# Optimization experiments

Hardware: AMD Instinct MI355X
Metric: run time of the kernel (lower is better)

## Reference

```python
import jax, jax.numpy as jnp
import numpy as np

B, C, T = 32, 64, 1024        # batch_size, in_channels, cycle_size
H, D = 2, 64                  # GATv2 heads, per-head dim (dim_h)
DIM2 = H * D                  # dim_h * 2 = 128
K = 9                         # temporal_kernel_size
N = B * T                     # graph nodes after flatten
E = 524288                    # edges (avg degree 16)
EPS = 1e-5


def bn3d(x, gamma, beta):
    # BatchNorm1d on [B, C, T] in training mode (batch statistics)
    mu = x.mean(axis=(0, 2), keepdims=True)
    var = x.var(axis=(0, 2), keepdims=True)
    xn = (x - mu) * jax.lax.rsqrt(var + EPS)
    return xn * gamma[None, :, None] + beta[None, :, None]


def bn2d(x, gamma, beta):
    # BatchNorm1d on [N, C] in training mode
    mu = x.mean(axis=0, keepdims=True)
    var = x.var(axis=0, keepdims=True)
    return (x - mu) * jax.lax.rsqrt(var + EPS) * gamma + beta


def conv1d_same(x, w, b):
    # x: [B, Cin, T], w: [Cout, Cin, K]
    y = jax.lax.conv_general_dilated(x, w, (1,), 'SAME',
                                     dimension_numbers=('NCH', 'OIH', 'NCH'))
    return y + b[None, :, None]


def gatv2(x, edge_index, wl, wr, att, bias):
    # PyG GATv2Conv defaults: heads=H, concat=True, leaky slope 0.2, self-loops
    loops = jnp.arange(N, dtype=edge_index.dtype)
    src = jnp.concatenate([edge_index[0], loops])
    dst = jnp.concatenate([edge_index[1], loops])
    xl = (x @ wl.T).reshape(N, H, D)   # source transform
    xr = (x @ wr.T).reshape(N, H, D)   # target transform
    m = jax.nn.leaky_relu(xl[src] + xr[dst], 0.2)        # [E+N, H, D]
    logits = jnp.einsum('ehd,hd->eh', m, att)            # [E+N, H]
    lmax = jax.ops.segment_max(logits, dst, num_segments=N)
    lmax = jax.lax.stop_gradient(jnp.where(jnp.isfinite(lmax), lmax, 0.0))
    p = jnp.exp(logits - lmax[dst])
    denom = jax.ops.segment_sum(p, dst, num_segments=N)  # >0: self-loops
    alpha = p / denom[dst]                               # softmax over in-edges
    out = jax.ops.segment_sum(xl[src] * alpha[:, :, None], dst, num_segments=N)
    return out.reshape(N, DIM2) + bias


def setup_inputs() -> dict:
    key = jax.random.key(0)
    ks = jax.random.split(key, 10)
    s = lambda k, shape: jax.random.normal(k, shape, jnp.float32) * 0.05
    return {
        'x': jax.random.normal(ks[0], (B, C, T), jnp.float32),
        'edge_index': jax.random.randint(ks[1], (2, E), 0, N, jnp.int32),
        'bn0_gamma': jnp.ones((C,), jnp.float32),
        'bn0_beta': jnp.zeros((C,), jnp.float32),
        'conv_w': s(ks[2], (DIM2, C, K)),
        'conv_b': s(ks[3], (DIM2,)),
        'gat_wl': s(ks[4], (DIM2, C)),
        'gat_wr': s(ks[5], (DIM2, C)),
        'gat_att': s(ks[6], (H, D)),
        'gat_bias': s(ks[7], (DIM2,)),
        'bn1_gamma': jnp.ones((DIM2,), jnp.float32),
        'bn1_beta': jnp.zeros((DIM2,), jnp.float32),
        'cheb_w': s(ks[8], (DIM2, DIM2)),
        'cheb_b': s(ks[9], (DIM2,)),
        'train': 0,
    }


def reference(x, edge_index, bn0_gamma, bn0_beta, conv_w, conv_b,
              gat_wl, gat_wr, gat_att, gat_bias, bn1_gamma, bn1_beta,
              cheb_w, cheb_b, train):
    x = bn3d(x, bn0_gamma, bn0_beta)                       # b0 (batch_size > 1)
    residual = jax.nn.relu(conv1d_same(x, conv_w, conv_b)) # skip_connection
    h = x.reshape(T * B, C)                                # flatten to nodes
    h = gatv2(h, edge_index, gat_wl, gat_wr, gat_att, gat_bias)
    h = jax.nn.relu(bn2d(h, bn1_gamma, bn1_beta))          # b1
    h = h.reshape(B, DIM2, T)
    h = residual + h
    # chain of views: (T*B,d) -> (B,d,T) -> (B,T,-1) -> (T*B,d); pure reshapes
    h = h.reshape(T * B, DIM2)
    h = h @ cheb_w.T + cheb_b                              # ChebConv K=1 == linear
    h = jax.nn.relu(bn2d(h, bn1_gamma, bn1_beta))          # b1 again
    h = h.reshape(B, DIM2, T)
    return residual + h                                    # dropout: identity (eval)
```

## Files before the change

kernel.cpp:

```cpp
#include <hip/hip_runtime.h>

#define DEVINL __device__ __forceinline__

constexpr int Bc = 32, Cc = 64, Tc = 1024, DIM2c = 128;
constexpr int Nn = Bc * Tc;
constexpr int Ec = 524288;

typedef __bf16 bf16x8 __attribute__((ext_vector_type(8)));
typedef float  f32x4  __attribute__((ext_vector_type(4)));

constexpr long O_RES   = 0;
constexpr long O_GOUT  = 4194304;
constexpr long O_XT    = 8388608;
constexpr long O_HBF   = 9437184;
constexpr long O_XLQ   = 10485760;
constexpr long O_XRQ   = 12582912;
constexpr long O_Z     = 16777216;
constexpr long O_WCBF  = 20971520;
constexpr long O_WLR   = 21008384;
constexpr long O_CHB   = 21016576;
constexpr long O_STAT  = 21024768;
constexpr long O_CUR   = 21025792;
constexpr long O_BUCK  = 21058560;

DEVINL float unpack_lo(unsigned v) { return __uint_as_float(v << 16); }
DEVINL float unpack_hi(unsigned v) { return __uint_as_float(v & 0xffff0000u); }
DEVINL unsigned bfb(float f) { return (__float_as_uint(f) + 0x8000u) >> 16; }
DEVINL unsigned pk2(float lo, float hi) {
    return ((__float_as_uint(hi) + 0x8000u) & 0xffff0000u) | bfb(lo);
}

__global__ __launch_bounds__(256) void setup(const float* __restrict__ x,
        const float* __restrict__ cw, const float* __restrict__ wl,
        const float* __restrict__ wr, const float* __restrict__ chw,
        const int* __restrict__ ei,
        __bf16* __restrict__ wcbf, __bf16* __restrict__ wlrbf,
        __bf16* __restrict__ chwbf,
        float* __restrict__ sum0, float* __restrict__ sq0,
        int* __restrict__ cursor, int* __restrict__ bucket) {
    int bid = blockIdx.x, tid = threadIdx.x;
    if (bid < 416) {
        int i = bid * 256 + tid;
        if (i < 73728) {
            int kk = i >> 13, co = (i >> 6) & 127, ci = i & 63;
            wcbf[i] = (__bf16)cw[co * 576 + ci * 9 + kk];
        } else if (i < 73728 + 16384) {
            int j = i - 73728;
            int r = j >> 6, c = j & 63;
            float v = (r < 128) ? wl[r * 64 + c] : wr[(r - 128) * 64 + c];
            wlrbf[j] = (__bf16)v;
        } else {
            int j = i - 73728 - 16384;
            chwbf[j] = (__bf16)chw[j];
        }
    } else if (bid < 672) {
        int pq = bid - 416;
        int c = pq & 63, q = pq >> 6;
        const float4* base = (const float4*)(x + (long)q * 8 * 65536 + (long)c * 1024);
        float s = 0.f, qq = 0.f;
        for (int i = tid; i < 2048; i += 256) {
            int b = i >> 8, t4 = i & 255;
            float4 v = base[b * 16384 + t4];
            s += v.x + v.y + v.z + v.w;
            qq = fmaf(v.x, v.x, qq); qq = fmaf(v.y, v.y, qq);
            qq = fmaf(v.z, v.z, qq); qq = fmaf(v.w, v.w, qq);
        }
        for (int off = 32; off; off >>= 1) { s += __shfl_down(s, off); qq += __shfl_down(qq, off); }
        __shared__ float ls[4], lq[4];
        int w = tid >> 6, lane = tid & 63;
        if (lane == 0) { ls[w] = s; lq[w] = qq; }
        __syncthreads();
        if (tid == 0) {
            unsafeAtomicAdd(sum0 + c, ls[0] + ls[1] + ls[2] + ls[3]);
            unsafeAtomicAdd(sq0 + c, lq[0] + lq[1] + lq[2] + lq[3]);
        }
    } else {
        int e = (bid - 672) * 256 + tid;
        int t = ei[Ec + e];
        int slot = atomicAdd(cursor + t, 1);
        bucket[t * 64 + slot] = ei[e];
    }
}

__global__ __launch_bounds__(256) void xprep(const float* __restrict__ x,
        const float* __restrict__ sum0, const float* __restrict__ sq0,
        const float* __restrict__ g0, const float* __restrict__ b0,
        __bf16* __restrict__ hbf, __bf16* __restrict__ xt) {
    __shared__ float lds[64][65];
    __shared__ float scs[64], shs[64];
    int tid = threadIdx.x;
    if (tid < 64) {
        float mu = sum0[tid] * (1.f / 32768.f);
        float var = sq0[tid] * (1.f / 32768.f) - mu * mu;
        float rs = rsqrtf(var + 1e-5f);
        float sc = rs * g0[tid];
        scs[tid] = sc; shs[tid] = b0[tid] - mu * sc;
    }
    __syncthreads();
    int t0 = blockIdx.x * 64;
    int b  = blockIdx.y;
    const float* xb = x + (long)b * 65536;
    for (int i = tid; i < 4096; i += 256) {
        int ci = i >> 6, tl = i & 63;
        float v = fmaf(xb[ci * 1024 + t0 + tl], scs[ci], shs[ci]);
        hbf[(long)b * 65536 + ci * 1024 + t0 + tl] = (__bf16)v;
        lds[ci][tl] = v;
    }
    __syncthreads();
    for (int i = tid; i < 4096; i += 256) {
        int t = i >> 6, ci = i & 63;
        xt[((long)b * 1024 + t0 + t) * 64 + ci] = (__bf16)lds[ci][t];
    }
}

constexpr int XS_STRIDE = 72;

DEVINL void conv_role(int cid, const __bf16* __restrict__ xt,
        const __bf16* __restrict__ wcbf, const float* __restrict__ cb,
        float* __restrict__ res, __bf16* xs) {
    int tid = threadIdx.x;
    int tbase = (cid & 7) * 128;
    int cohalf = (cid >> 3) & 1;
    int b = cid >> 4;
    const uint2* xg = (const uint2*)(xt + (long)b * 65536);
    for (int i = tid; i < 136 * 16; i += 256) {
        int row = i >> 4, c4 = i & 15;
        int t = tbase + row - 4;
        uint2 v; v.x = 0u; v.y = 0u;
        if ((unsigned)t < 1024u) v = xg[t * 16 + c4];
        *(uint2*)(xs + row * XS_STRIDE + c4 * 4) = v;
    }
    __syncthreads();
    int wv = tid >> 6, lane = tid & 63;
    int col = lane & 15, q = lane >> 4;
    int co0 = cohalf * 64 + wv * 16;
    bf16x8 af[18];
    #pragma unroll
    for (int kk = 0; kk < 9; kk++)
        #pragma unroll
        for (int ks = 0; ks < 2; ks++)
            af[kk * 2 + ks] = *(const bf16x8*)(wcbf +
                ((long)kk * 8192 + (long)(co0 + col) * 64 + ks * 32 + q * 8));
    float bi0 = cb[co0 + q * 4], bi1 = cb[co0 + q * 4 + 1];
    float bi2 = cb[co0 + q * 4 + 2], bi3 = cb[co0 + q * 4 + 3];
    for (int nt = 0; nt < 8; nt++) {
        int t0 = tbase + nt * 16;
        f32x4 acc; acc[0] = bi0; acc[1] = bi1; acc[2] = bi2; acc[3] = bi3;
        #pragma unroll
        for (int kk = 0; kk < 9; kk++) {
            const __bf16* rp = xs + (nt * 16 + col + kk) * XS_STRIDE + q * 8;
            #pragma unroll
            for (int ks = 0; ks < 2; ks++) {
                bf16x8 bfx = *(const bf16x8*)(rp + ks * 32);
                acc = __builtin_amdgcn_mfma_f32_16x16x32_bf16(af[kk * 2 + ks], bfx, acc, 0, 0, 0);
            }
        }
        long ob = (long)b * 131072 + (long)(co0 + q * 4) * 1024 + t0 + col;
        res[ob]        = fmaxf(acc[0], 0.f);
        res[ob + 1024] = fmaxf(acc[1], 0.f);
        res[ob + 2048] = fmaxf(acc[2], 0.f);
        res[ob + 3072] = fmaxf(acc[3], 0.f);
    }
}

DEVINL void gemm1_role(int mb, const __bf16* __restrict__ hbf,
        const __bf16* __restrict__ wlrbf,
        unsigned short* __restrict__ xl16, unsigned short* __restrict__ xr16) {
    int wv = threadIdx.x >> 6, lane = threadIdx.x & 63;
    int col = lane & 15, q = lane >> 4;
    int d0 = wv * 16;
    long mbase = (long)mb * 64;
    bf16x8 bfr[4][2];
    #pragma unroll
    for (int t = 0; t < 4; t++) {
        int j = d0 + t * 64 + col;
        #pragma unroll
        for (int ks = 0; ks < 2; ks++)
            bfr[t][ks] = *(const bf16x8*)(wlrbf + (long)j * 64 + ks * 32 + q * 8);
    }
    int d = d0 + col;
    for (int mt = 0; mt < 4; mt++) {
        long r0 = mbase + mt * 16;
        bf16x8 a0 = *(const bf16x8*)(hbf + (r0 + col) * 64 + q * 8);
        bf16x8 a1 = *(const bf16x8*)(hbf + (r0 + col) * 64 + 32 + q * 8);
        f32x4 acc[4];
        #pragma unroll
        for (int t = 0; t < 4; t++) { acc[t][0] = 0.f; acc[t][1] = 0.f; acc[t][2] = 0.f; acc[t][3] = 0.f; }
        #pragma unroll
        for (int t = 0; t < 4; t++) {
            acc[t] = __builtin_amdgcn_mfma_f32_16x16x32_bf16(a0, bfr[t][0], acc[t], 0, 0, 0);
            acc[t] = __builtin_amdgcn_mfma_f32_16x16x32_bf16(a1, bfr[t][1], acc[t], 0, 0, 0);
        }
        #pragma unroll
        for (int reg = 0; reg < 4; reg++) {
            long rb = (r0 + q * 4 + reg) * 128;
            xl16[rb + d]      = (unsigned short)bfb(acc[0][reg]);
            xl16[rb + 64 + d] = (unsigned short)bfb(acc[1][reg]);
            xr16[rb + d]      = (unsigned short)bfb(acc[2][reg]);
            xr16[rb + 64 + d] = (unsigned short)bfb(acc[3][reg]);
        }
    }
}

__global__ __launch_bounds__(256) void conv_gemm1(const __bf16* __restrict__ xt,
        const __bf16* __restrict__ wcbf, const float* __restrict__ cb,
        float* __restrict__ res, const __bf16* __restrict__ hbf,
        const __bf16* __restrict__ wlrbf,
        unsigned* __restrict__ xlq, unsigned* __restrict__ xrq) {
    __shared__ __align__(16) __bf16 xs[136 * XS_STRIDE];
    int bid = blockIdx.x;
    if (bid & 1) gemm1_role(bid >> 1, hbf, wlrbf, (unsigned short*)xlq, (unsigned short*)xrq);
    else conv_role(bid >> 1, xt, wcbf, cb, res, xs);
}

__global__ __launch_bounds__(256) void gat_agg(const uint4* __restrict__ xlq4,
        const uint4* __restrict__ xrq4,
        const int* __restrict__ cursor, const int* __restrict__ bucket,
        const float* __restrict__ att, unsigned* __restrict__ goutb) {
    int wid = (blockIdx.x * 256 + threadIdx.x) >> 6;
    int lane = threadIdx.x & 63;
    int g = lane >> 3, j = lane & 7;
    float av[16];
    #pragma unroll
    for (int k = 0; k < 16; k++) av[k] = att[16 * j + k];
    uint4 r0v = xrq4[(long)wid * 16 + j * 2];
    uint4 r1v = xrq4[(long)wid * 16 + j * 2 + 1];
    float xr[16];
    {
        unsigned ru[8] = {r0v.x, r0v.y, r0v.z, r0v.w, r1v.x, r1v.y, r1v.z, r1v.w};
        #pragma unroll
        for (int k = 0; k < 8; k++) { xr[2*k] = unpack_lo(ru[k]); xr[2*k+1] = unpack_hi(ru[k]); }
    }
    int cnt = cursor[wid];
    int s_all = bucket[wid * 64 + lane];
    float acc[16];
    #pragma unroll
    for (int k = 0; k < 16; k++) acc[k] = 0.f;
    float den = 0.f;
    int nit = (cnt + 8) >> 3;
    int sp = __shfl(s_all, g);
    sp = (g < cnt) ? sp : wid;
    uint4 p0 = xlq4[(long)sp * 16 + j * 2];
    uint4 p1 = xlq4[(long)sp * 16 + j * 2 + 1];
    for (int it = 0; it < nit; it++) {
        uint4 c0 = p0, c1 = p1;
        int icur = it * 8 + g;
        int inext = icur + 8;
        if (it + 1 < nit) {
            int sn = __shfl(s_all, inext & 63);
            sn = (inext < cnt) ? sn : wid;
            p0 = xlq4[(long)sn * 16 + j * 2];
            p1 = xlq4[(long)sn * 16 + j * 2 + 1];
        }
        unsigned uu[8] = {c0.x, c0.y, c0.z, c0.w, c1.x, c1.y, c1.z, c1.w};
        float xl[16];
        float w = 0.f;
        #pragma unroll
        for (int k = 0; k < 8; k++) {
            float lo = unpack_lo(uu[k]), hi = unpack_hi(uu[k]);
            xl[2*k] = lo; xl[2*k+1] = hi;
            float s0 = lo + xr[2*k]; s0 = fmaxf(s0, 0.2f * s0);
            float s1 = hi + xr[2*k+1]; s1 = fmaxf(s1, 0.2f * s1);
            w = fmaf(s1, av[2*k+1], fmaf(s0, av[2*k], w));
        }
        w += __shfl_xor(w, 1); w += __shfl_xor(w, 2);
        float e2 = (icur <= cnt) ? __expf(w) : 0.f;
        den += e2;
        #pragma unroll
        for (int k = 0; k < 16; k++) acc[k] = fmaf(e2, xl[k], acc[k]);
    }
    #pragma unroll
    for (int m = 8; m <= 32; m <<= 1) {
        den += __shfl_xor(den, m);
        #pragma unroll
        for (int k = 0; k < 16; k++) acc[k] += __shfl_xor(acc[k], m);
    }
    float rn = __builtin_amdgcn_rcpf(den);
    if (g == 0) {
        #pragma unroll
        for (int c = 0; c < 2; c++) {
            uint4 o;
            o.x = pk2(acc[8*c]     * rn, acc[8*c + 1] * rn);
            o.y = pk2(acc[8*c + 2] * rn, acc[8*c + 3] * rn);
            o.z = pk2(acc[8*c + 4] * rn, acc[8*c + 5] * rn);
            o.w = pk2(acc[8*c + 6] * rn, acc[8*c + 7] * rn);
            *(uint4*)(goutb + (long)wid * 64 + 8 * j + 4 * c) = o;
        }
    }
}

__global__ __launch_bounds__(256) void bn_stats_bf(const unsigned* __restrict__ G,
        float* __restrict__ sum, float* __restrict__ sq) {
    int c = threadIdx.x & 63, sub = threadIdx.x >> 6;
    int r0 = blockIdx.x * 256;
    float sl = 0.f, sh = 0.f, ql = 0.f, qh = 0.f;
    for (int r = r0 + sub; r < r0 + 256; r += 4) {
        unsigned v = G[(long)r * 64 + c];
        float lo = unpack_lo(v), hi = unpack_hi(v);
        sl += lo; ql = fmaf(lo, lo, ql);
        sh += hi; qh = fmaf(hi, hi, qh);
    }
    __shared__ float A[256], B[256], C[256], D[256];
    A[threadIdx.x] = sl; B[threadIdx.x] = sh;
    C[threadIdx.x] = ql; D[threadIdx.x] = qh;
    __syncthreads();
    if (threadIdx.x < 64) {
        int t = threadIdx.x;
        float s_lo = A[t] + A[t + 64] + A[t + 128] + A[t + 192];
        float s_hi = B[t] + B[t + 64] + B[t + 128] + B[t + 192];
        float q_lo = C[t] + C[t + 64] + C[t + 128] + C[t + 192];
        float q_hi = D[t] + D[t + 64] + D[t + 128] + D[t + 192];
        unsafeAtomicAdd(sum + 2 * t,     s_lo);
        unsafeAtomicAdd(sum + 2 * t + 1, s_hi);
        unsafeAtomicAdd(sq  + 2 * t,     q_lo);
        unsafeAtomicAdd(sq  + 2 * t + 1, q_hi);
    }
}

__global__ __launch_bounds__(256) void cheb_fused(const unsigned* __restrict__ goutb,
        const float* __restrict__ res, const float* __restrict__ sum1,
        const float* __restrict__ sq1, const float* __restrict__ g1,
        const float* __restrict__ b1, const __bf16* __restrict__ chwbf,
        unsigned* __restrict__ zb, float* __restrict__ sum2, float* __restrict__ sq2) {
    __shared__ unsigned xs[64 * 68];
    __shared__ float scs[128], shs[128], cs[128], cq[128];
    int tid = threadIdx.x;
    if (tid < 128) {
        float mu = sum1[tid] * (1.f / 32768.f);
        float var = sq1[tid] * (1.f / 32768.f) - mu * mu;
        float rs = rsqrtf(var + 1e-5f);
        float sc = rs * g1[tid];
        scs[tid] = sc; shs[tid] = b1[tid] - mu * sc;
        cs[tid] = 0.f;
    } else cq[tid - 128] = 0.f;
    __syncthreads();
    long r0 = (long)blockIdx.x * 64;
    for (int i = tid; i < 2048; i += 256) {
        int row = i >> 5, c4 = i & 31;
        long gidx = (r0 + row) * 32 + c4;
        uint2 gv = ((const uint2*)goutb)[gidx];
        float4 r = ((const float4*)res)[gidx];
        int f0 = c4 * 4;
        float v0 = unpack_lo(gv.x), v1 = unpack_hi(gv.x);
        float v2 = unpack_lo(gv.y), v3 = unpack_hi(gv.y);
        float o0 = r.x + fmaxf(fmaf(v0, scs[f0],     shs[f0]),     0.f);
        float o1 = r.y + fmaxf(fmaf(v1, scs[f0 + 1], shs[f0 + 1]), 0.f);
        float o2 = r.z + fmaxf(fmaf(v2, scs[f0 + 2], shs[f0 + 2]), 0.f);
        float o3 = r.w + fmaxf(fmaf(v3, scs[f0 + 3], shs[f0 + 3]), 0.f);
        xs[row * 68 + c4 * 2]     = pk2(o0, o1);
        xs[row * 68 + c4 * 2 + 1] = pk2(o2, o3);
    }
    __syncthreads();
    int wv = tid >> 6, lane = tid & 63;
    int col = lane & 15, q = lane >> 4;
    bf16x8 bfr[2][4];
    #pragma unroll
    for (int t = 0; t < 2; t++) {
        int jj = wv * 16 + t * 64 + col;
        #pragma unroll
        for (int ks = 0; ks < 4; ks++)
            bfr[t][ks] = *(const bf16x8*)(chwbf + (long)jj * 128 + ks * 32 + q * 8);
    }
    float ls0 = 0.f, ls1 = 0.f, lq0 = 0.f, lq1 = 0.f;
    bool evenc = (col & 1) == 0;
    int fpair0 = (wv * 16 + col) >> 1;
    for (int mt = 0; mt < 4; mt++) {
        const __bf16* ap = (const __bf16*)xs + (mt * 16 + col) * 136;
        bf16x8 a[4];
        #pragma unroll
        for (int ks = 0; ks < 4; ks++)
            a[ks] = *(const bf16x8*)(ap + ks * 32 + q * 8);
        f32x4 acc[2];
        #pragma unroll
        for (int t = 0; t < 2; t++) { acc[t][0] = 0.f; acc[t][1] = 0.f; acc[t][2] = 0.f; acc[t][3] = 0.f; }
        #pragma unroll
        for (int t = 0; t < 2; t++)
            #pragma unroll
            for (int ks = 0; ks < 4; ks++)
                acc[t] = __builtin_amdgcn_mfma_f32_16x16x32_bf16(a[ks], bfr[t][ks], acc[t], 0, 0, 0);
        #pragma unroll
        for (int reg = 0; reg < 4; reg++) {
            float v0 = acc[0][reg], v1 = acc[1][reg];
            ls0 += v0; lq0 = fmaf(v0, v0, lq0);
            ls1 += v1; lq1 = fmaf(v1, v1, lq1);
            float n0 = __shfl_xor(v0, 1);
            float n1 = __shfl_xor(v1, 1);
            if (evenc) {
                long zrow = (r0 + mt * 16 + q * 4 + reg) * 64;
                zb[zrow + fpair0]      = pk2(v0, n0);
                zb[zrow + 32 + fpair0] = pk2(v1, n1);
            }
        }
    }
    int j0 = wv * 16 + col;
    atomicAdd(&cs[j0], ls0);      atomicAdd(&cs[j0 + 64], ls1);
    atomicAdd(&cq[j0], lq0);      atomicAdd(&cq[j0 + 64], lq1);
    __syncthreads();
    if (tid < 128) unsafeAtomicAdd(sum2 + tid, cs[tid]);
    else unsafeAtomicAdd(sq2 + tid - 128, cq[tid - 128]);
}

__global__ __launch_bounds__(256) void bn_res(const unsigned* __restrict__ zb,
        const float* __restrict__ res, const float* __restrict__ sum,
        const float* __restrict__ sq, const float* __restrict__ g,
        const float* __restrict__ bta, float* __restrict__ out) {
    __shared__ float scs[128], shs[128];
    int tid = threadIdx.x;
    if (tid < 128) {
        float mu = sum[tid] * (1.f / 32768.f);
        float var = sq[tid] * (1.f / 32768.f) - mu * mu;
        float rs = rsqrtf(var + 1e-5f);
        float sc = rs * g[tid];
        scs[tid] = sc; shs[tid] = bta[tid] - mu * sc;
    }
    __syncthreads();
    int idx = blockIdx.x * 256 + tid;
    int f0 = (idx & 31) * 4;
    uint2 zv = ((const uint2*)zb)[idx];
    float4 r = ((const float4*)res)[idx];
    float v0 = unpack_lo(zv.x), v1 = unpack_hi(zv.x);
    float v2 = unpack_lo(zv.y), v3 = unpack_hi(zv.y);
    float4 o;
    o.x = r.x + fmaxf(fmaf(v0, scs[f0],     shs[f0]),     0.f);
    o.y = r.y + fmaxf(fmaf(v1, scs[f0 + 1], shs[f0 + 1]), 0.f);
    o.z = r.z + fmaxf(fmaf(v2, scs[f0 + 2], shs[f0 + 2]), 0.f);
    o.w = r.w + fmaxf(fmaf(v3, scs[f0 + 3], shs[f0 + 3]), 0.f);
    ((float4*)out)[idx] = o;
}

extern "C" void kernel_launch(void* const* d_in, const int* in_sizes, int n_in,
                              void* d_out, int out_size, void* d_ws, size_t ws_size,
                              hipStream_t stream) {
    const float* x   = (const float*)d_in[0];
    const int*   ei  = (const int*)d_in[1];
    const float* g0  = (const float*)d_in[2];
    const float* b0  = (const float*)d_in[3];
    const float* cw  = (const float*)d_in[4];
    const float* cb  = (const float*)d_in[5];
    const float* wl  = (const float*)d_in[6];
    const float* wr  = (const float*)d_in[7];
    const float* att = (const float*)d_in[8];
    const float* g1  = (const float*)d_in[10];
    const float* b1  = (const float*)d_in[11];
    const float* chw = (const float*)d_in[12];
    float* out = (float*)d_out;

    float* ws = (float*)d_ws;
    float*    res   = ws + O_RES;
    unsigned* goutb = (unsigned*)(ws + O_GOUT);
    __bf16*   xt    = (__bf16*)(ws + O_XT);
    __bf16*   hbf   = (__bf16*)(ws + O_HBF);
    unsigned* xlq   = (unsigned*)(ws + O_XLQ);
    unsigned* xrq   = (unsigned*)(ws + O_XRQ);
    unsigned* zb    = (unsigned*)(ws + O_Z);
    __bf16*   wcbf  = (__bf16*)(ws + O_WCBF);
    __bf16*   wlrbf = (__bf16*)(ws + O_WLR);
    __bf16*   chwbf = (__bf16*)(ws + O_CHB);
    float*    st    = ws + O_STAT;
    int*      cursor = (int*)(ws + O_CUR);
    int*      bucket = (int*)(ws + O_BUCK);
    float *sum0 = st,       *sq0 = st + 64;
    float *sum1 = st + 128, *sq1 = st + 256;
    float *sum2 = st + 384, *sq2 = st + 512;

    hipMemsetAsync(st, 0, (size_t)(1024 + 32768) * 4, stream);

    setup<<<2720, 256, 0, stream>>>(x, cw, wl, wr, chw, ei,
                                    wcbf, wlrbf, chwbf, sum0, sq0, cursor, bucket);
    xprep<<<dim3(16, 32), 256, 0, stream>>>(x, sum0, sq0, g0, b0, hbf, xt);
    conv_gemm1<<<1024, 256, 0, stream>>>(xt, wcbf, cb, res, hbf, wlrbf, xlq, xrq);
    gat_agg<<<8192, 256, 0, stream>>>((const uint4*)xlq, (const uint4*)xrq,
                                      cursor, bucket, att, goutb);
    bn_stats_bf<<<128, 256, 0, stream>>>(goutb, sum1, sq1);
    cheb_fused<<<512, 256, 0, stream>>>(goutb, res, sum1, sq1, g1, b1, chwbf,
                                        zb, sum2, sq2);
    bn_res<<<4096, 256, 0, stream>>>(zb, res, sum2, sq2, g1, b1, out);
}
```

Before: 223.3 us.

## Fuse BN0 into GEMM1 and conv loaders, co-schedule conv with GAT aggregation

Removes the separate xprep kernel and its bf16 intermediates (hbf, xt). The GATv2 projection GEMM now reads fp32 x and applies BN0 on the fly into LDS. The temporal conv also normalizes x while staging its halo tile, and conv blocks share a launch with the GAT aggregation blocks instead of the GEMM. This cuts one kernel launch and a round trip through intermediate buffers, and lets conv overlap the gather-heavy GAT work. The cost is a strided per-channel transposing LDS write in the conv loader, recomputation of BN0 scale factors per block, and bn_stats using twice as many smaller blocks.

```diff
diff --git a/kernel.cpp b/kernel.cpp
--- a/kernel.cpp
+++ b/kernel.cpp
@@ -11,8 +11,6 @@
 
 constexpr long O_RES   = 0;
 constexpr long O_GOUT  = 4194304;
-constexpr long O_XT    = 8388608;
-constexpr long O_HBF   = 9437184;
 constexpr long O_XLQ   = 10485760;
 constexpr long O_XRQ   = 12582912;
 constexpr long O_Z     = 16777216;
@@ -82,58 +80,113 @@
     }
 }
 
-__global__ __launch_bounds__(256) void xprep(const float* __restrict__ x,
+__global__ __launch_bounds__(256) void gemm1_bn0(const float* __restrict__ x,
         const float* __restrict__ sum0, const float* __restrict__ sq0,
         const float* __restrict__ g0, const float* __restrict__ b0,
-        __bf16* __restrict__ hbf, __bf16* __restrict__ xt) {
-    __shared__ float lds[64][65];
-    __shared__ float scs[64], shs[64];
+        const __bf16* __restrict__ wlrbf,
+        unsigned short* __restrict__ xl16, unsigned short* __restrict__ xr16) {
+    __shared__ __align__(16) __bf16 as_[64 * 72];
     int tid = threadIdx.x;
-    if (tid < 64) {
-        float mu = sum0[tid] * (1.f / 32768.f);
-        float var = sq0[tid] * (1.f / 32768.f) - mu * mu;
-        float rs = rsqrtf(var + 1e-5f);
-        float sc = rs * g0[tid];
-        scs[tid] = sc; shs[tid] = b0[tid] - mu * sc;
-    }
-    __syncthreads();
-    int t0 = blockIdx.x * 64;
-    int b  = blockIdx.y;
-    const float* xb = x + (long)b * 65536;
-    for (int i = tid; i < 4096; i += 256) {
-        int ci = i >> 6, tl = i & 63;
-        float v = fmaf(xb[ci * 1024 + t0 + tl], scs[ci], shs[ci]);
-        hbf[(long)b * 65536 + ci * 1024 + t0 + tl] = (__bf16)v;
-        lds[ci][tl] = v;
-    }
-    __syncthreads();
-    for (int i = tid; i < 4096; i += 256) {
-        int t = i >> 6, ci = i & 63;
-        xt[((long)b * 1024 + t0 + t) * 64 + ci] = (__bf16)lds[ci][t];
+    int mb = blockIdx.x;
+    int b = mb >> 4, ci0 = (mb & 15) * 4;
+    const float4* x4 = (const float4*)(x + (long)b * 65536 + (long)ci0 * 1024);
+    #pragma unroll
+    for (int it = 0; it < 4; it++) {
+        int ci = ci0 + it;
+        float mu = sum0[ci] * (1.f / 32768.f);
+        float var = sq0[ci] * (1.f / 32768.f) - mu * mu;
+        float sc = rsqrtf(var + 1e-5f) * g0[ci];
+        float sh = b0[ci] - mu * sc;
+        float4 v = x4[it * 256 + tid];
+        int row = it * 16 + (tid >> 4);
+        int col = (tid & 15) * 4;
+        __bf16* p = as_ + row * 72 + col;
+        p[0] = (__bf16)fmaf(v.x, sc, sh);
+        p[1] = (__bf16)fmaf(v.y, sc, sh);
+        p[2] = (__bf16)fmaf(v.z, sc, sh);
+        p[3] = (__bf16)fmaf(v.w, sc, sh);
+    }
+    __syncthreads();
+    int wv = tid >> 6, lane = tid & 63;
+    int col = lane & 15, q = lane >> 4;
+    int d0 = wv * 16;
+    long mbase = (long)mb * 64;
+    bf16x8 bfr[4][2];
+    #pragma unroll
+    for (int t = 0; t < 4; t++) {
+        int j = d0 + t * 64 + col;
+        #pragma unroll
+        for (int ks = 0; ks < 2; ks++)
+            bfr[t][ks] = *(const bf16x8*)(wlrbf + (long)j * 64 + ks * 32 + q * 8);
+    }
+    int d = d0 + col;
+    for (int mt = 0; mt < 4; mt++) {
+        const __bf16* ap = as_ + (mt * 16 + col) * 72;
+        bf16x8 a0 = *(const bf16x8*)(ap + q * 8);
+        bf16x8 a1 = *(const bf16x8*)(ap + 32 + q * 8);
+        f32x4 acc[4];
+        #pragma unroll
+        for (int t = 0; t < 4; t++) { acc[t][0] = 0.f; acc[t][1] = 0.f; acc[t][2] = 0.f; acc[t][3] = 0.f; }
+        #pragma unroll
+        for (int t = 0; t < 4; t++) {
+            acc[t] = __builtin_amdgcn_mfma_f32_16x16x32_bf16(a0, bfr[t][0], acc[t], 0, 0, 0);
+            acc[t] = __builtin_amdgcn_mfma_f32_16x16x32_bf16(a1, bfr[t][1], acc[t], 0, 0, 0);
+        }
+        long r0 = mbase + mt * 16;
+        #pragma unroll
+        for (int reg = 0; reg < 4; reg++) {
+            long rb = (r0 + q * 4 + reg) * 128;
+            xl16[rb + d]      = (unsigned short)bfb(acc[0][reg]);
+            xl16[rb + 64 + d] = (unsigned short)bfb(acc[1][reg]);
+            xr16[rb + d]      = (unsigned short)bfb(acc[2][reg]);
+            xr16[rb + 64 + d] = (unsigned short)bfb(acc[3][reg]);
+        }
     }
 }
 
 constexpr int XS_STRIDE = 72;
 
-DEVINL void conv_role(int cid, const __bf16* __restrict__ xt,
+DEVINL void conv_role(int cid, const float* __restrict__ x,
+        const float* __restrict__ sum0, const float* __restrict__ sq0,
+        const float* __restrict__ g0, const float* __restrict__ b0,
         const __bf16* __restrict__ wcbf, const float* __restrict__ cb,
-        float* __restrict__ res, __bf16* xs) {
+        float* __restrict__ res, __bf16* xs, float* scs, float* shs) {
     int tid = threadIdx.x;
     int tbase = (cid & 7) * 128;
     int cohalf = (cid >> 3) & 1;
     int b = cid >> 4;
-    const uint2* xg = (const uint2*)(xt + (long)b * 65536);
-    for (int i = tid; i < 136 * 16; i += 256) {
-        int row = i >> 4, c4 = i & 15;
-        int t = tbase + row - 4;
-        uint2 v; v.x = 0u; v.y = 0u;
-        if ((unsigned)t < 1024u) v = xg[t * 16 + c4];
-        *(uint2*)(xs + row * XS_STRIDE + c4 * 4) = v;
-    }
-    __syncthreads();
-    int wv = tid >> 6, lane = tid & 63;
+    if (tid < 64) {
+        float mu = sum0[tid] * (1.f / 32768.f);
+        float var = sq0[tid] * (1.f / 32768.f) - mu * mu;
+        float sc = rsqrtf(var + 1e-5f) * g0[tid];
+        scs[tid] = sc; shs[tid] = b0[tid] - mu * sc;
+    }
+    __syncthreads();
+    int w = tid >> 6, lane = tid & 63;
+    const float* xb = x + (long)b * 65536;
+    for (int cc = 0; cc < 16; cc++) {
+        int ci = w * 16 + cc;
+        float sc = scs[ci], sh = shs[ci];
+        const float* xp = xb + ci * 1024 + tbase - 4;
+        #pragma unroll
+        for (int rp = 0; rp < 2; rp++) {
+            int rr = rp * 64 + lane;
+            int t = tbase - 4 + rr;
+            float v = 0.f;
+            if ((unsigned)t < 1024u) v = fmaf(xp[rr], sc, sh);
+            xs[rr * XS_STRIDE + ci] = (__bf16)v;
+        }
+        if (lane < 8) {
+            int rr = 128 + lane;
+            int t = tbase - 4 + rr;
+            float v = 0.f;
+            if ((unsigned)t < 1024u) v = fmaf(xp[rr], sc, sh);
+            xs[rr * XS_STRIDE + ci] = (__bf16)v;
+        }
+    }
+    __syncthreads();
     int col = lane & 15, q = lane >> 4;
-    int co0 = cohalf * 64 + wv * 16;
+    int co0 = cohalf * 64 + w * 16;
     bf16x8 af[18];
     #pragma unroll
     for (int kk = 0; kk < 9; kk++)
@@ -163,61 +216,10 @@
     }
 }
 
-DEVINL void gemm1_role(int mb, const __bf16* __restrict__ hbf,
-        const __bf16* __restrict__ wlrbf,
-        unsigned short* __restrict__ xl16, unsigned short* __restrict__ xr16) {
-    int wv = threadIdx.x >> 6, lane = threadIdx.x & 63;
-    int col = lane & 15, q = lane >> 4;
-    int d0 = wv * 16;
-    long mbase = (long)mb * 64;
-    bf16x8 bfr[4][2];
-    #pragma unroll
-    for (int t = 0; t < 4; t++) {
-        int j = d0 + t * 64 + col;
-        #pragma unroll
-        for (int ks = 0; ks < 2; ks++)
-            bfr[t][ks] = *(const bf16x8*)(wlrbf + (long)j * 64 + ks * 32 + q * 8);
-    }
-    int d = d0 + col;
-    for (int mt = 0; mt < 4; mt++) {
-        long r0 = mbase + mt * 16;
-        bf16x8 a0 = *(const bf16x8*)(hbf + (r0 + col) * 64 + q * 8);
-        bf16x8 a1 = *(const bf16x8*)(hbf + (r0 + col) * 64 + 32 + q * 8);
-        f32x4 acc[4];
-        #pragma unroll
-        for (int t = 0; t < 4; t++) { acc[t][0] = 0.f; acc[t][1] = 0.f; acc[t][2] = 0.f; acc[t][3] = 0.f; }
-        #pragma unroll
-        for (int t = 0; t < 4; t++) {
-            acc[t] = __builtin_amdgcn_mfma_f32_16x16x32_bf16(a0, bfr[t][0], acc[t], 0, 0, 0);
-            acc[t] = __builtin_amdgcn_mfma_f32_16x16x32_bf16(a1, bfr[t][1], acc[t], 0, 0, 0);
-        }
-        #pragma unroll
-        for (int reg = 0; reg < 4; reg++) {
-            long rb = (r0 + q * 4 + reg) * 128;
-            xl16[rb + d]      = (unsigned short)bfb(acc[0][reg]);
-            xl16[rb + 64 + d] = (unsigned short)bfb(acc[1][reg]);
-            xr16[rb + d]      = (unsigned short)bfb(acc[2][reg]);
-            xr16[rb + 64 + d] = (unsigned short)bfb(acc[3][reg]);
-        }
-    }
-}
-
-__global__ __launch_bounds__(256) void conv_gemm1(const __bf16* __restrict__ xt,
-        const __bf16* __restrict__ wcbf, const float* __restrict__ cb,
-        float* __restrict__ res, const __bf16* __restrict__ hbf,
-        const __bf16* __restrict__ wlrbf,
-        unsigned* __restrict__ xlq, unsigned* __restrict__ xrq) {
-    __shared__ __align__(16) __bf16 xs[136 * XS_STRIDE];
-    int bid = blockIdx.x;
-    if (bid & 1) gemm1_role(bid >> 1, hbf, wlrbf, (unsigned short*)xlq, (unsigned short*)xrq);
-    else conv_role(bid >> 1, xt, wcbf, cb, res, xs);
-}
-
-__global__ __launch_bounds__(256) void gat_agg(const uint4* __restrict__ xlq4,
+DEVINL void gat_role(int wid, const uint4* __restrict__ xlq4,
         const uint4* __restrict__ xrq4,
         const int* __restrict__ cursor, const int* __restrict__ bucket,
         const float* __restrict__ att, unsigned* __restrict__ goutb) {
-    int wid = (blockIdx.x * 256 + threadIdx.x) >> 6;
     int lane = threadIdx.x & 63;
     int g = lane >> 3, j = lane & 7;
     float av[16];
@@ -289,12 +291,30 @@
     }
 }
 
+__global__ __launch_bounds__(256) void conv_gat(const float* __restrict__ x,
+        const float* __restrict__ sum0, const float* __restrict__ sq0,
+        const float* __restrict__ g0, const float* __restrict__ b0,
+        const __bf16* __restrict__ wcbf, const float* __restrict__ cb,
+        float* __restrict__ res,
+        const uint4* __restrict__ xlq4, const uint4* __restrict__ xrq4,
+        const int* __restrict__ cursor, const int* __restrict__ bucket,
+        const float* __restrict__ att, unsigned* __restrict__ goutb) {
+    __shared__ __align__(16) __bf16 xs[136 * XS_STRIDE];
+    __shared__ float scs[64], shs[64];
+    int bid = blockIdx.x;
+    if (bid < 512)
+        conv_role(bid, x, sum0, sq0, g0, b0, wcbf, cb, res, xs, scs, shs);
+    else
+        gat_role(((bid - 512) * 256 + (int)threadIdx.x) >> 6,
+                 xlq4, xrq4, cursor, bucket, att, goutb);
+}
+
 __global__ __launch_bounds__(256) void bn_stats_bf(const unsigned* __restrict__ G,
         float* __restrict__ sum, float* __restrict__ sq) {
     int c = threadIdx.x & 63, sub = threadIdx.x >> 6;
-    int r0 = blockIdx.x * 256;
+    int r0 = blockIdx.x * 128;
     float sl = 0.f, sh = 0.f, ql = 0.f, qh = 0.f;
-    for (int r = r0 + sub; r < r0 + 256; r += 4) {
+    for (int r = r0 + sub; r < r0 + 128; r += 4) {
         unsigned v = G[(long)r * 64 + c];
         float lo = unpack_lo(v), hi = unpack_hi(v);
         sl += lo; ql = fmaf(lo, lo, ql);
@@ -322,7 +342,7 @@
         const float* __restrict__ sq1, const float* __restrict__ g1,
         const float* __restrict__ b1, const __bf16* __restrict__ chwbf,
         unsigned* __restrict__ zb, float* __restrict__ sum2, float* __restrict__ sq2) {
-    __shared__ unsigned xs[64 * 68];
+    __shared__ unsigned xsu[64 * 68];
     __shared__ float scs[128], shs[128], cs[128], cq[128];
     int tid = threadIdx.x;
     if (tid < 128) {
@@ -347,8 +367,8 @@
         float o1 = r.y + fmaxf(fmaf(v1, scs[f0 + 1], shs[f0 + 1]), 0.f);
         float o2 = r.z + fmaxf(fmaf(v2, scs[f0 + 2], shs[f0 + 2]), 0.f);
         float o3 = r.w + fmaxf(fmaf(v3, scs[f0 + 3], shs[f0 + 3]), 0.f);
-        xs[row * 68 + c4 * 2]     = pk2(o0, o1);
-        xs[row * 68 + c4 * 2 + 1] = pk2(o2, o3);
+        xsu[row * 68 + c4 * 2]     = pk2(o0, o1);
+        xsu[row * 68 + c4 * 2 + 1] = pk2(o2, o3);
     }
     __syncthreads();
     int wv = tid >> 6, lane = tid & 63;
@@ -365,7 +385,7 @@
     bool evenc = (col & 1) == 0;
     int fpair0 = (wv * 16 + col) >> 1;
     for (int mt = 0; mt < 4; mt++) {
-        const __bf16* ap = (const __bf16*)xs + (mt * 16 + col) * 136;
+        const __bf16* ap = (const __bf16*)xsu + (mt * 16 + col) * 136;
         bf16x8 a[4];
         #pragma unroll
         for (int ks = 0; ks < 4; ks++)
@@ -448,8 +468,6 @@
     float* ws = (float*)d_ws;
     float*    res   = ws + O_RES;
     unsigned* goutb = (unsigned*)(ws + O_GOUT);
-    __bf16*   xt    = (__bf16*)(ws + O_XT);
-    __bf16*   hbf   = (__bf16*)(ws + O_HBF);
     unsigned* xlq   = (unsigned*)(ws + O_XLQ);
     unsigned* xrq   = (unsigned*)(ws + O_XRQ);
     unsigned* zb    = (unsigned*)(ws + O_Z);
@@ -467,11 +485,12 @@
 
     setup<<<2720, 256, 0, stream>>>(x, cw, wl, wr, chw, ei,
                                     wcbf, wlrbf, chwbf, sum0, sq0, cursor, bucket);
-    xprep<<<dim3(16, 32), 256, 0, stream>>>(x, sum0, sq0, g0, b0, hbf, xt);
-    conv_gemm1<<<1024, 256, 0, stream>>>(xt, wcbf, cb, res, hbf, wlrbf, xlq, xrq);
-    gat_agg<<<8192, 256, 0, stream>>>((const uint4*)xlq, (const uint4*)xrq,
-                                      cursor, bucket, att, goutb);
-    bn_stats_bf<<<128, 256, 0, stream>>>(goutb, sum1, sq1);
+    gemm1_bn0<<<512, 256, 0, stream>>>(x, sum0, sq0, g0, b0, wlrbf,
+                                       (unsigned short*)xlq, (unsigned short*)xrq);
+    conv_gat<<<8704, 256, 0, stream>>>(x, sum0, sq0, g0, b0, wcbf, cb, res,
+                                       (const uint4*)xlq, (const uint4*)xrq,
+                                       cursor, bucket, att, goutb);
+    bn_stats_bf<<<256, 256, 0, stream>>>(goutb, sum1, sq1);
     cheb_fused<<<512, 256, 0, stream>>>(goutb, res, sum1, sq1, g1, b1, chwbf,
                                         zb, sum2, sq2);
     bn_res<<<4096, 256, 0, stream>>>(zb, res, sum2, sq2, g1, b1, out);
```

New measurement: 219.2 us. About the same (-1.9%).
